# Kernel optimization log

Hardware: AMD Instinct MI355X
Metric: run time of the kernel (lower is better)

## Reference

```python
import jax, jax.numpy as jnp
import numpy as np

N, E, D, T, R, H = 50000, 400000, 256, 3, 6, 4
DK = D // H          # 64, d_k = out_dim // n_heads
OUT = H * DK         # 256
LN_EPS = 1e-5


def setup_inputs() -> dict:
    key = jax.random.key(0)
    ks = jax.random.split(key, 16)
    std = 0.02  # initializer_range in HGTClassfication._init_weights
    f32 = jnp.float32
    inp = {
        "x": jax.random.normal(ks[0], (N, D), f32),
        "Wk": jax.random.normal(ks[1], (T, D, OUT), f32) * std,
        "bk": jnp.zeros((T, OUT), f32),
        "Wq": jax.random.normal(ks[2], (T, D, OUT), f32) * std,
        "bq": jnp.zeros((T, OUT), f32),
        "Wv": jax.random.normal(ks[3], (T, D, OUT), f32) * std,
        "bv": jnp.zeros((T, OUT), f32),
        "Wa": jax.random.normal(ks[4], (T, OUT, OUT), f32) * std,
        "ba": jnp.zeros((T, OUT), f32),
        "rel_pri": jnp.ones((R, H), f32),
        "rel_att": jax.random.normal(ks[5], (R, H, DK, DK), f32) * (1.0 / np.sqrt(DK)),
        "rel_msg": jax.random.normal(ks[6], (R, H, DK, DK), f32) * (1.0 / np.sqrt(DK)),
        "skip": jnp.ones((T,), f32),
        "ln_g": jnp.ones((T, OUT), f32),
        "ln_b": jnp.zeros((T, OUT), f32),
        "node_type": jax.random.randint(ks[7], (N,), 0, T),
        "edge_src": jax.random.randint(ks[8], (E,), 0, N),
        "edge_dst": jax.random.randint(ks[9], (E,), 0, N),
        "edge_type": jax.random.randint(ks[10], (E,), 0, R),
        "n_heads": H,
    }
    return inp


def reference(x, Wk, bk, Wq, bq, Wv, bv, Wa, ba, rel_pri, rel_att, rel_msg,
              skip, ln_g, ln_b, node_type, edge_src, edge_dst, edge_type, n_heads):
    n, d = x.shape
    r, h = rel_pri.shape
    dk = rel_att.shape[-1]
    out_dim = h * dk
    ar = jnp.arange(n)

    def typed_linear(inp_, W, b):
        # per-node-type Linear: compute for all T types, pick by node_type
        y = jnp.einsum('ni,tio->tno', inp_, W) + b[:, None, :]
        return y[node_type, ar]

    k = typed_linear(x, Wk, bk).reshape(n, h, dk)
    q = typed_linear(x, Wq, bq).reshape(n, h, dk)
    v = typed_linear(x, Wv, bv).reshape(n, h, dk)

    # relation-specific transforms (done on nodes, gathered per edge: N*R << E*R work)
    k_rel = jnp.einsum('nhd,rhde->rnhe', k, rel_att)   # [R,N,H,dk]
    v_rel = jnp.einsum('nhd,rhde->rnhe', v, rel_msg)   # [R,N,H,dk]
    key_e = k_rel[edge_type, edge_src]                 # [E,H,dk]
    val_e = v_rel[edge_type, edge_src]                 # [E,H,dk]

    att = (q[edge_dst] * key_e).sum(-1) * rel_pri[edge_type] / jnp.sqrt(jnp.float32(dk))  # [E,H]

    # per-(dst, etype) mailbox softmax + weighted sum (DGL reduce per canonical etype)
    seg = edge_dst * r + edge_type
    S = n * r
    amax = jax.ops.segment_max(att, seg, num_segments=S)
    amax = jax.lax.stop_gradient(jnp.where(jnp.isfinite(amax), amax, 0.0))
    ex = jnp.exp(att - amax[seg])
    denom = jax.ops.segment_sum(ex, seg, num_segments=S)
    w = ex / denom[seg]                                # [E,H]
    hsum = jax.ops.segment_sum(w[:, :, None] * val_e, seg, num_segments=S)  # [S,H,dk]
    cnt = jax.ops.segment_sum(jnp.ones((seg.shape[0],), x.dtype), seg, num_segments=S)

    # cross_reducer='mean' over relations that delivered messages
    t_rel = hsum.reshape(n, r, out_dim)
    present = cnt.reshape(n, r) > 0
    nrel = jnp.maximum(present.sum(-1), 1).astype(x.dtype)
    t = (t_rel * present[..., None].astype(x.dtype)).sum(1) / nrel[:, None]

    trans = typed_linear(t, Wa, ba)
    alpha = jax.nn.sigmoid(skip)[node_type][:, None]
    out = trans * alpha + x * (1.0 - alpha)

    mu = out.mean(-1, keepdims=True)
    var = out.var(-1, keepdims=True)
    normed = (out - mu) * jax.lax.rsqrt(var + LN_EPS) * ln_g[node_type] + ln_b[node_type]

    # nodes with no incoming edges keep their input feature (no 't' in DGL data)
    has_msg = present.any(-1)[:, None]
    return jnp.where(has_msg, normed, x)
```

## Files before the change

kernel.cpp:

```cpp
#include <hip/hip_runtime.h>
#include <hip/hip_bf16.h>


#define NN 50000
#define EE 400000
#define TN 3
#define RN 6
#define HN 4
#define SS (NN * RN)
#define NCHUNK 293
#define CD 16
#define LCAP 640

typedef __hip_bfloat16 bf16;
typedef unsigned short u16;
using bf16x8 = __attribute__((ext_vector_type(8))) __bf16;
using f32x4  = __attribute__((ext_vector_type(4))) float;

__device__ __forceinline__ float b2f(bf16 h) { return __bfloat162float(h); }
__device__ __forceinline__ float busf(u16 u) { return __uint_as_float((unsigned)u << 16); }
__device__ __forceinline__ float blo(unsigned u) { return __uint_as_float(u << 16); }
__device__ __forceinline__ float bhi(unsigned u) { return __uint_as_float(u & 0xffff0000u); }
__device__ __forceinline__ u16 f2us(float f) {
    unsigned u = __float_as_uint(f);
    return (u16)((u + 0x7fffu + ((u >> 16) & 1u)) >> 16);
}
__device__ __forceinline__ float ld(const void* p, long i, int f) {
    return f ? ((const float*)p)[i] : b2f(((const bf16*)p)[i]);
}

__global__ __launch_bounds__(256) void detect_dtype(const void* __restrict__ x,
                                                    int* __restrict__ flag) {
    __shared__ int cnt_s;
    if (threadIdx.x == 0) cnt_s = 0;
    __syncthreads();
    const u16* p = (const u16*)x;
    int c = 0;
    for (int i = threadIdx.x; i < 8192; i += 256) {
        int expo = (p[i] >> 7) & 0xFF;
        if (expo >= 0x97) ++c;
    }
    atomicAdd(&cnt_s, c);
    __syncthreads();
    if (threadIdx.x == 0) *flag = (cnt_s > 64) ? 1 : 0;
}

__global__ __launch_bounds__(256) void prep(const void* __restrict__ rel_att,
        const void* __restrict__ rel_msg,
        const void* __restrict__ Wk, const void* __restrict__ Wq,
        const void* __restrict__ Wv, const void* __restrict__ Wa,
        const void* __restrict__ x, const int* __restrict__ node_type,
        const int* __restrict__ edst, const int* __restrict__ etype,
        const int* __restrict__ flag,
        u16* __restrict__ MTa, u16* __restrict__ MTm,
        u16* __restrict__ WallT, u16* __restrict__ WaT,
        u16* __restrict__ xb,
        int* __restrict__ lists, int* __restrict__ cnts,
        unsigned* __restrict__ cnt) {
    int b = blockIdx.x;
    int t = threadIdx.x;
    if (b < 48) {
        int f = *flag;
        int m = b;
        long base = (long)(m % 24) * 4096;
        if (m < 24) {
            for (int it = 0; it < 16; ++it) {
                int idx = it * 256 + t;
                MTa[base + idx] = f2us(ld(rel_att, base + idx, f));
            }
        } else {
            for (int it = 0; it < 16; ++it) {
                int idx = it * 256 + t;
                int d = idx >> 6, j = idx & 63;
                MTm[base + (j << 6) + d] = f2us(ld(rel_msg, base + idx, f));
            }
        }
    } else if (b < 3120) {
        int f = *flag;
        int m = b - 48;
        if (m < 2304) {
            int ty = m / 768, o3 = m % 768;
            int sec = o3 >> 8, o = o3 & 255;
            const void* W = (sec == 0) ? Wk : (sec == 1) ? Wq : Wv;
            WallT[(size_t)ty * 768 * 256 + (size_t)o3 * 256 + t] =
                f2us(ld(W, (long)ty * 65536 + (long)t * 256 + o, f));
        } else {
            int mm = m - 2304;
            int ty = mm / 256, o = mm % 256;
            WaT[(size_t)ty * 65536 + (size_t)o * 256 + t] =
                f2us(ld(Wa, (long)ty * 65536 + (long)t * 256 + o, f));
        }
    } else if (b < 15620) {
        int f = *flag;
        long i = ((long)(b - 3120) * 256 + t) * 4;
        if (i < (long)NN * 256) {
            if (f) {
                float4 v = *(const float4*)((const float*)x + i);
                ushort4 p; p.x = f2us(v.x); p.y = f2us(v.y); p.z = f2us(v.z); p.w = f2us(v.w);
                *(ushort4*)(xb + i) = p;
            } else {
                *(ushort4*)(xb + i) = *(const ushort4*)((const u16*)x + i);
            }
        }
    } else if (b < 15816) {
        __shared__ int lc[TN], lbase[TN];
        if (t < TN) lc[t] = 0;
        __syncthreads();
        int n = (b - 15620) * 256 + t;
        int pos = -1, ty = 0;
        if (n < NN) {
            ty = node_type[n];
            pos = atomicAdd(&lc[ty], 1);
        }
        __syncthreads();
        if (t < TN) lbase[t] = atomicAdd(&cnts[t], lc[t]);
        __syncthreads();
        if (n < NN) lists[ty * NN + lbase[ty] + pos] = n;
    } else {
        int e = (b - 15816) * 256 + t;
        if (e < EE) atomicAdd(&cnt[etype[e] * NN + edst[e]], 1u);
    }
}

__global__ __launch_bounds__(256) void scanA(const unsigned* __restrict__ cnt,
                                             unsigned* __restrict__ csums) {
    __shared__ unsigned s[256];
    int b = blockIdx.x, t = threadIdx.x;
    int s0 = b * 1024 + t * 4;
    unsigned v = 0;
    if (s0 + 3 < SS) { uint4 u = *(const uint4*)&cnt[s0]; v = u.x + u.y + u.z + u.w; }
    else { for (int j = 0; j < 4; ++j) if (s0 + j < SS) v += cnt[s0 + j]; }
    s[t] = v;
    __syncthreads();
    for (int st = 128; st > 0; st >>= 1) {
        if (t < st) s[t] += s[t + st];
        __syncthreads();
    }
    if (t == 0) csums[b] = s[0];
}

__global__ __launch_bounds__(256) void scanB(unsigned* __restrict__ csums,
                                             int* __restrict__ base) {
    __shared__ unsigned s[512];
    int t = threadIdx.x;
    unsigned a = (t < NCHUNK) ? csums[t] : 0u;
    unsigned b = (256 + t < NCHUNK) ? csums[256 + t] : 0u;
    s[t] = a; s[256 + t] = b;
    __syncthreads();
    for (int st = 1; st < 512; st <<= 1) {
        unsigned x0 = (t >= st) ? s[t - st] : 0u;
        unsigned x1 = (256 + t >= st) ? s[256 + t - st] : 0u;
        __syncthreads();
        s[t] += x0; s[256 + t] += x1;
        __syncthreads();
    }
    if (t < NCHUNK) csums[t] = s[t] - a;
    if (256 + t < NCHUNK) csums[256 + t] = s[256 + t] - b;
    if (t == 0) base[SS] = (int)s[NCHUNK - 1];
}

__global__ __launch_bounds__(256) void scanC(const unsigned* __restrict__ cnt,
        const unsigned* __restrict__ csums, int* __restrict__ base) {
    __shared__ unsigned s[256];
    int b = blockIdx.x, t = threadIdx.x;
    int s0 = b * 1024 + t * 4;
    unsigned vs[4] = {0u, 0u, 0u, 0u};
    if (s0 + 3 < SS) { uint4 u = *(const uint4*)&cnt[s0]; vs[0]=u.x; vs[1]=u.y; vs[2]=u.z; vs[3]=u.w; }
    else { for (int j = 0; j < 4; ++j) if (s0 + j < SS) vs[j] = cnt[s0 + j]; }
    unsigned v = vs[0] + vs[1] + vs[2] + vs[3];
    s[t] = v;
    __syncthreads();
    for (int st = 1; st < 256; st <<= 1) {
        unsigned x = (t >= st) ? s[t - st] : 0u;
        __syncthreads();
        s[t] += x;
        __syncthreads();
    }
    unsigned run = csums[b] + s[t] - v;
    for (int j = 0; j < 4; ++j) {
        if (s0 + j < SS) { base[s0 + j] = (int)run; run += vs[j]; }
    }
}

__global__ __launch_bounds__(256) void scatter_edges(const int* __restrict__ edst,
        const int* __restrict__ etype, const int* __restrict__ base,
        unsigned* __restrict__ cnt, int* __restrict__ sorted) {
    int e = blockIdx.x * 256 + threadIdx.x;
    if (e >= EE) return;
    int seg = etype[e] * NN + edst[e];
    unsigned old = atomicSub(&cnt[seg], 1u);
    sorted[base[seg] + (int)old - 1] = e;
}

__global__ __launch_bounds__(512, 2) void k1_mfma(const u16* __restrict__ xb,
        const u16* __restrict__ WallT,
        const void* __restrict__ bk, const void* __restrict__ bq,
        const void* __restrict__ bv,
        const int* __restrict__ lists, const int* __restrict__ cnts,
        const int* __restrict__ flag,
        u16* __restrict__ kb, u16* __restrict__ qb, u16* __restrict__ vb) {
    int f = *flag;
    int tt = blockIdx.x % TN, tile = blockIdx.x / TN;
    int cnt = cnts[tt];
    int start = tile * 64;
    if (start >= cnt) return;
    __shared__ int nl[64];
    __shared__ __align__(16) u16 xs[64][280];
    __shared__ __align__(16) float bias_s[768];
    int t = threadIdx.x;
    if (t < 64) nl[t] = (start + t < cnt) ? lists[tt * NN + start + t] : -1;
    if (t < 256) {
        bias_s[t]       = ld(bk, tt * 256 + t, f);
        bias_s[256 + t] = ld(bq, tt * 256 + t, f);
        bias_s[512 + t] = ld(bv, tt * 256 + t, f);
    }
    __syncthreads();
    {
        int i = t >> 4, g = t & 15;
        #pragma unroll
        for (int i2 = 0; i2 < 2; ++i2) {
            int row = i + i2 * 32;
            int node = nl[row];
            uint4 a = {0, 0, 0, 0}, b = {0, 0, 0, 0};
            if (node >= 0) {
                const uint4* src = (const uint4*)(xb + (size_t)node * 256 + g * 16);
                a = src[0]; b = src[1];
            }
            *(uint4*)&xs[row][g * 16] = a;
            *(uint4*)&xs[row][g * 16 + 8] = b;
        }
    }
    __syncthreads();
    int w = t >> 6, lane = t & 63, ln = lane & 15, quad = lane >> 4;
    const u16* Wt = WallT + (size_t)tt * 768 * 256;
    f32x4 acc[6][4];
    #pragma unroll
    for (int j = 0; j < 6; ++j)
        #pragma unroll
        for (int g = 0; g < 4; ++g)
            acc[j][g] = (f32x4){0.f, 0.f, 0.f, 0.f};
    for (int kt = 0; kt < 8; ++kt) {
        bf16x8 A[6];
        #pragma unroll
        for (int jt = 0; jt < 6; ++jt)
            A[jt] = *(const bf16x8*)(Wt + (size_t)(w * 96 + jt * 16 + ln) * 256 + kt * 32 + quad * 8);
        bf16x8 B[4];
        #pragma unroll
        for (int g = 0; g < 4; ++g)
            B[g] = *(const bf16x8*)&xs[g * 16 + ln][kt * 32 + quad * 8];
        #pragma unroll
        for (int jt = 0; jt < 6; ++jt)
            #pragma unroll
            for (int g = 0; g < 4; ++g)
                acc[jt][g] = __builtin_amdgcn_mfma_f32_16x16x32_bf16(A[jt], B[g], acc[jt][g], 0, 0, 0);
    }
    #pragma unroll
    for (int jt = 0; jt < 6; ++jt) {
        int jc = w * 96 + jt * 16 + quad * 4;
        float4 bi = *(const float4*)&bias_s[jc];
        int sec = jc >> 8, o = jc & 255;
        u16* basep = (sec == 0 ? kb : sec == 1 ? qb : vb);
        #pragma unroll
        for (int g = 0; g < 4; ++g) {
            int node = nl[g * 16 + ln];
            if (node >= 0) {
                ushort4 p;
                p.x = f2us(acc[jt][g][0] + bi.x); p.y = f2us(acc[jt][g][1] + bi.y);
                p.z = f2us(acc[jt][g][2] + bi.z); p.w = f2us(acc[jt][g][3] + bi.w);
                *(ushort4*)(basep + (size_t)node * 256 + o) = p;
            }
        }
    }
}

__global__ __launch_bounds__(256) void k2k4(const u16* __restrict__ kb,
        const u16* __restrict__ qb, const u16* __restrict__ vb,
        const u16* __restrict__ MTa, const u16* __restrict__ MTm,
        const void* __restrict__ rel_pri,
        const int* __restrict__ sorted, const int* __restrict__ base,
        const int* __restrict__ esrc, const int* __restrict__ edst,
        const int* __restrict__ flag,
        u16* __restrict__ attex_g, float* __restrict__ tacc) {
    int f = *flag;
    int c0 = blockIdx.x * CD;
    int nd = min(CD, NN - c0);
    __shared__ float attL[LCAP];
    __shared__ int srcL[LCAP];
    __shared__ float denomL[CD * HN];
    __shared__ int sb_[CD + 1];
    __shared__ __align__(16) u16 qL[CD][264];
    __shared__ __align__(16) u16 qrs[CD][264];
    int t = threadIdx.x;
    int w = t >> 6, lane = t & 63, ln = lane & 15, quad = lane >> 4;
    {
        int i = t >> 4, g = t & 15;
        uint4 a0 = {0,0,0,0}, a1 = {0,0,0,0};
        if (i < nd) {
            const uint4* src = (const uint4*)(qb + (size_t)(c0 + i) * 256 + g * 16);
            a0 = src[0]; a1 = src[1];
        }
        *(uint4*)&qL[i][g * 16] = a0;
        *(uint4*)&qL[i][g * 16 + 8] = a1;
    }
    f32x4 accF[4];
    #pragma unroll
    for (int m = 0; m < 4; ++m) accF[m] = (f32x4){0.f, 0.f, 0.f, 0.f};

    for (int r = 0; r < RN; ++r) {
        if (t < CD * HN) denomL[t] = 0.f;
        if (t <= nd) sb_[t] = base[r * NN + c0 + t];
        __syncthreads();
        long mtbase = (long)(r * HN + w) * 4096;
        {
            bf16x8 B0 = *(const bf16x8*)&qL[ln][w * 64 + quad * 8];
            bf16x8 B1 = *(const bf16x8*)&qL[ln][w * 64 + quad * 8 + 32];
            #pragma unroll
            for (int mt = 0; mt < 4; ++mt) {
                const u16* ap = MTa + mtbase + (mt * 16 + ln) * 64 + quad * 8;
                bf16x8 A0 = *(const bf16x8*)(ap);
                bf16x8 A1 = *(const bf16x8*)(ap + 32);
                f32x4 acc = {0.f, 0.f, 0.f, 0.f};
                acc = __builtin_amdgcn_mfma_f32_16x16x32_bf16(A0, B0, acc, 0, 0, 0);
                acc = __builtin_amdgcn_mfma_f32_16x16x32_bf16(A1, B1, acc, 0, 0, 0);
                int jc = w * 64 + mt * 16 + quad * 4;
                ushort4 pq;
                pq.x = f2us(acc[0]); pq.y = f2us(acc[1]);
                pq.z = f2us(acc[2]); pq.w = f2us(acc[3]);
                *(ushort4*)&qrs[ln][jc] = pq;
            }
        }
        __syncthreads();
        int b0 = sb_[0], nE = sb_[nd] - b0;
        for (int i = t; i < nE * 4; i += 256) {
            int ei = i >> 2;
            int e = sorted[b0 + ei];
            int h = i & 3;
            int s = esrc[e], dv = edst[e] - c0;
            if (h == 0 && ei < LCAP) srcL[ei] = s;
            const uint4* kp = (const uint4*)(kb + (size_t)s * 256 + h * 64);
            const uint4* qp = (const uint4*)&qrs[dv][h * 64];
            float dot = 0.f;
            #pragma unroll
            for (int ii = 0; ii < 8; ++ii) {
                uint4 a = kp[ii], b = qp[ii];
                dot += blo(a.x) * blo(b.x) + bhi(a.x) * bhi(b.x);
                dot += blo(a.y) * blo(b.y) + bhi(a.y) * bhi(b.y);
                dot += blo(a.z) * blo(b.z) + bhi(a.z) * bhi(b.z);
                dot += blo(a.w) * blo(b.w) + bhi(a.w) * bhi(b.w);
            }
            float attv = dot * ld(rel_pri, r * HN + h, f) * 0.125f;
            attv = fminf(fmaxf(attv, -50.f), 50.f);
            float ex = expf(attv);
            if (i < LCAP) attL[i] = ex;
            else attex_g[(size_t)b0 * 4 + i] = f2us(ex);
            atomicAdd(&denomL[dv * HN + h], ex);
        }
        __syncthreads();
        {
            int half = lane >> 5, lane32 = lane & 31;
            int h = lane32 >> 3;
            for (int i2 = w * 2 + half; i2 < nd; i2 += 8) {
                int sb = sb_[i2], se = sb_[i2 + 1];
                float a0=0.f,a1=0.f,a2=0.f,a3=0.f,a4=0.f,a5=0.f,a6=0.f,a7=0.f;
                if (se > sb) {
                    float inv = 1.f / denomL[i2 * HN + h];
                    for (int idx = sb; idx < se; ++idx) {
                        int rel = idx - b0;
                        int li2 = rel * 4 + h;
                        float wgt = ((li2 < LCAP) ? attL[li2]
                                     : busf(attex_g[(size_t)idx * 4 + h])) * inv;
                        int s = (rel < LCAP) ? srcL[rel] : esrc[sorted[idx]];
                        uint4 v = *(const uint4*)(vb + (size_t)s * 256 + lane32 * 8);
                        a0 += wgt * blo(v.x); a1 += wgt * bhi(v.x);
                        a2 += wgt * blo(v.y); a3 += wgt * bhi(v.y);
                        a4 += wgt * blo(v.z); a5 += wgt * bhi(v.z);
                        a6 += wgt * blo(v.w); a7 += wgt * bhi(v.w);
                    }
                }
                u16 pv8[8];
                pv8[0]=f2us(a0); pv8[1]=f2us(a1); pv8[2]=f2us(a2); pv8[3]=f2us(a3);
                pv8[4]=f2us(a4); pv8[5]=f2us(a5); pv8[6]=f2us(a6); pv8[7]=f2us(a7);
                *(uint4*)&qrs[i2][lane32 * 8] = *(const uint4*)pv8;
            }
        }
        __syncthreads();
        {
            bf16x8 B0 = *(const bf16x8*)&qrs[ln][w * 64 + quad * 8];
            bf16x8 B1 = *(const bf16x8*)&qrs[ln][w * 64 + quad * 8 + 32];
            #pragma unroll
            for (int mt = 0; mt < 4; ++mt) {
                const u16* mp = MTm + mtbase + (mt * 16 + ln) * 64 + quad * 8;
                bf16x8 A0 = *(const bf16x8*)(mp);
                bf16x8 A1 = *(const bf16x8*)(mp + 32);
                accF[mt] = __builtin_amdgcn_mfma_f32_16x16x32_bf16(A0, B0, accF[mt], 0, 0, 0);
                accF[mt] = __builtin_amdgcn_mfma_f32_16x16x32_bf16(A1, B1, accF[mt], 0, 0, 0);
            }
        }
    }
    if (ln < nd) {
        #pragma unroll
        for (int mt = 0; mt < 4; ++mt) {
            int jc = w * 64 + mt * 16 + quad * 4;
            float4 v = {accF[mt][0], accF[mt][1], accF[mt][2], accF[mt][3]};
            *(float4*)(tacc + (long)(c0 + ln) * 256 + jc) = v;
        }
    }
}

__global__ __launch_bounds__(512, 4) void k5_fused(const void* __restrict__ x,
        const float* __restrict__ tacc, const u16* __restrict__ WaT,
        const void* __restrict__ ba, const void* __restrict__ skip,
        const void* __restrict__ ln_g, const void* __restrict__ ln_b,
        const int* __restrict__ base,
        const int* __restrict__ lists, const int* __restrict__ cnts,
        const int* __restrict__ flag, void* out) {
    int f = *flag;
    int tt = blockIdx.x % TN, tile = blockIdx.x / TN;
    int cnt = cnts[tt];
    int start = tile * 64;
    if (start >= cnt) return;
    __shared__ int nl[64];
    __shared__ float invs[64];
    __shared__ int hasv[64];
    __shared__ __align__(16) u16 xs[64][280];
    __shared__ __align__(16) float ba_s[256], lnG_s[256], lnB_s[256];
    __shared__ float red1[64][8], red2[64][8];
    __shared__ float mu_[64], rs_[64];
    int t = threadIdx.x;
    if (t < 64) {
        int node = (start + t < cnt) ? lists[tt * NN + start + t] : -1;
        nl[t] = node;
        int nrel = 0;
        if (node >= 0) {
            #pragma unroll
            for (int r = 0; r < RN; ++r)
                nrel += (base[r * NN + node + 1] > base[r * NN + node]) ? 1 : 0;
        }
        hasv[t] = nrel;
        invs[t] = (nrel > 0) ? 1.f / (float)nrel : 1.f;
    }
    if (t < 256) {
        ba_s[t]  = ld(ba,   tt * 256 + t, f);
        lnG_s[t] = ld(ln_g, tt * 256 + t, f);
        lnB_s[t] = ld(ln_b, tt * 256 + t, f);
    }
    __syncthreads();
    {
        int i = t >> 3, g8 = t & 7;
        int node = nl[i];
        float inv = invs[i];
        int o0 = g8 * 32;
        u16 tmp[32];
        if (node >= 0) {
            const float* src = tacc + (long)node * 256 + o0;
            #pragma unroll
            for (int j = 0; j < 8; ++j) {
                float4 v = *(const float4*)(src + j * 4);
                tmp[j*4+0] = f2us(v.x * inv); tmp[j*4+1] = f2us(v.y * inv);
                tmp[j*4+2] = f2us(v.z * inv); tmp[j*4+3] = f2us(v.w * inv);
            }
        } else {
            #pragma unroll
            for (int j = 0; j < 32; ++j) tmp[j] = 0;
        }
        #pragma unroll
        for (int j = 0; j < 4; ++j)
            *(uint4*)&xs[i][o0 + j * 8] = ((const uint4*)tmp)[j];
    }
    __syncthreads();
    int w = t >> 6, lane = t & 63, ln = lane & 15, quad = lane >> 4;
    const u16* Wt = WaT + (size_t)tt * 65536;
    f32x4 acc[2][4];
    #pragma unroll
    for (int j = 0; j < 2; ++j)
        #pragma unroll
        for (int g = 0; g < 4; ++g)
            acc[j][g] = (f32x4){0.f, 0.f, 0.f, 0.f};
    for (int kt = 0; kt < 8; ++kt) {
        bf16x8 A[2];
        #pragma unroll
        for (int jt = 0; jt < 2; ++jt)
            A[jt] = *(const bf16x8*)(Wt + (size_t)(w * 32 + jt * 16 + ln) * 256 + kt * 32 + quad * 8);
        bf16x8 B[4];
        #pragma unroll
        for (int g = 0; g < 4; ++g)
            B[g] = *(const bf16x8*)&xs[g * 16 + ln][kt * 32 + quad * 8];
        #pragma unroll
        for (int jt = 0; jt < 2; ++jt)
            #pragma unroll
            for (int g = 0; g < 4; ++g)
                acc[jt][g] = __builtin_amdgcn_mfma_f32_16x16x32_bf16(A[jt], B[g], acc[jt][g], 0, 0, 0);
    }
    float sk = ld(skip, tt, f);
    float alpha = 1.f / (1.f + expf(-sk));
    float p1[4] = {0.f, 0.f, 0.f, 0.f}, p2[4] = {0.f, 0.f, 0.f, 0.f};
    #pragma unroll
    for (int g = 0; g < 4; ++g) {
        int node = nl[g * 16 + ln];
        if (node < 0) continue;
        #pragma unroll
        for (int jt = 0; jt < 2; ++jt) {
            int jc = w * 32 + jt * 16 + quad * 4;
            float4 bi = *(const float4*)&ba_s[jc];
            long xo = (long)node * 256 + jc;
            float xv[4];
            if (f) {
                float4 v = *(const float4*)((const float*)x + xo);
                xv[0] = v.x; xv[1] = v.y; xv[2] = v.z; xv[3] = v.w;
            } else {
                ushort4 v = *(const ushort4*)((const u16*)x + xo);
                xv[0] = busf(v.x); xv[1] = busf(v.y); xv[2] = busf(v.z); xv[3] = busf(v.w);
            }
            #pragma unroll
            for (int rg = 0; rg < 4; ++rg) {
                float ov = acc[jt][g][rg] + ((const float*)&bi)[rg];
                ov = ov * alpha + xv[rg] * (1.f - alpha);
                acc[jt][g][rg] = ov;
                p1[g] += ov; p2[g] += ov * ov;
            }
        }
    }
    #pragma unroll
    for (int g = 0; g < 4; ++g) {
        p1[g] += __shfl_xor(p1[g], 16); p1[g] += __shfl_xor(p1[g], 32);
        p2[g] += __shfl_xor(p2[g], 16); p2[g] += __shfl_xor(p2[g], 32);
    }
    if (quad == 0) {
        #pragma unroll
        for (int g = 0; g < 4; ++g) {
            red1[g * 16 + ln][w] = p1[g];
            red2[g * 16 + ln][w] = p2[g];
        }
    }
    __syncthreads();
    if (t < 64) {
        float s1 = 0.f, s2 = 0.f;
        #pragma unroll
        for (int j = 0; j < 8; ++j) { s1 += red1[t][j]; s2 += red2[t][j]; }
        float mu = s1 * (1.f / 256.f);
        float ms = s2 * (1.f / 256.f);
        float var = fmaxf(ms - mu * mu, 0.f);
        mu_[t] = mu; rs_[t] = rsqrtf(var + 1e-5f);
    }
    __syncthreads();
    #pragma unroll
    for (int g = 0; g < 4; ++g) {
        int li = g * 16 + ln;
        int node = nl[li];
        if (node < 0) continue;
        if (hasv[li] > 0) {
            float mu = mu_[li], rs = rs_[li];
            #pragma unroll
            for (int jt = 0; jt < 2; ++jt) {
                int jc = w * 32 + jt * 16 + quad * 4;
                float4 gg = *(const float4*)&lnG_s[jc];
                float4 bb = *(const float4*)&lnB_s[jc];
                long oo = (long)node * 256 + jc;
                float r0 = (acc[jt][g][0] - mu) * rs * gg.x + bb.x;
                float r1 = (acc[jt][g][1] - mu) * rs * gg.y + bb.y;
                float r2 = (acc[jt][g][2] - mu) * rs * gg.z + bb.z;
                float r3 = (acc[jt][g][3] - mu) * rs * gg.w + bb.w;
                if (f) { float4 v = {r0, r1, r2, r3}; *(float4*)((float*)out + oo) = v; }
                else   { ushort4 v; v.x = f2us(r0); v.y = f2us(r1); v.z = f2us(r2); v.w = f2us(r3);
                         *(ushort4*)((u16*)out + oo) = v; }
            }
        } else {
            #pragma unroll
            for (int jt = 0; jt < 2; ++jt) {
                int jc = w * 32 + jt * 16 + quad * 4;
                long oo = (long)node * 256 + jc;
                if (f) { *(float4*)((float*)out + oo) = *(const float4*)((const float*)x + oo); }
                else   { *(ushort4*)((u16*)out + oo) = *(const ushort4*)((const u16*)x + oo); }
            }
        }
    }
}

extern "C" void kernel_launch(void* const* d_in, const int* in_sizes, int n_in,
                              void* d_out, int out_size, void* d_ws, size_t ws_size,
                              hipStream_t stream) {
    const void* x       = d_in[0];
    const void* Wk      = d_in[1];
    const void* bk      = d_in[2];
    const void* Wq      = d_in[3];
    const void* bq      = d_in[4];
    const void* Wv      = d_in[5];
    const void* bv      = d_in[6];
    const void* Wa      = d_in[7];
    const void* ba      = d_in[8];
    const void* rel_pri = d_in[9];
    const void* rel_att = d_in[10];
    const void* rel_msg = d_in[11];
    const void* skip    = d_in[12];
    const void* ln_g    = d_in[13];
    const void* ln_b    = d_in[14];
    const int* node_type = (const int*)d_in[15];
    const int* edge_src  = (const int*)d_in[16];
    const int* edge_dst  = (const int*)d_in[17];
    const int* edge_type = (const int*)d_in[18];
    char* w = (char*)d_ws;

    u16*      kb     = (u16*)(w);
    u16*      qb     = (u16*)(w + 25600000);
    u16*      vb     = (u16*)(w + 51200000);
    float*    tacc   = (float*)(w + 76800000);
    u16*      xb     = (u16*)(w + 76800000);
    u16*      attex  = (u16*)(w + 128000000);
    int*      sorted = (int*)(w + 131200000);
    int*      base   = (int*)(w + 132800000);
    int*      nlists = (int*)(w + 134000064);
    u16*      MTa    = (u16*)(w + 134600064);
    u16*      MTm    = (u16*)(w + 134796672);
    u16*      WallT  = (u16*)(w + 134993280);
    u16*      WaT    = (u16*)(w + 136172928);
    unsigned* cnt    = (unsigned*)(w + 136566144);
    int*      ncnts  = (int*)(w + 137766144);
    int*      flag   = (int*)(w + 137766208);
    unsigned* csums  = (unsigned*)(w + 137766272);

    hipMemsetAsync(w + 136566144, 0, 1201408, stream);

    detect_dtype<<<dim3(1), dim3(256), 0, stream>>>(x, flag);
    prep<<<dim3(17379), dim3(256), 0, stream>>>(
        rel_att, rel_msg, Wk, Wq, Wv, Wa, x, node_type, edge_dst, edge_type,
        flag, MTa, MTm, WallT, WaT, xb, nlists, ncnts, cnt);
    scanA<<<dim3(NCHUNK), dim3(256), 0, stream>>>(cnt, csums);
    scanB<<<dim3(1), dim3(256), 0, stream>>>(csums, base);
    scanC<<<dim3(NCHUNK), dim3(256), 0, stream>>>(cnt, csums, base);
    scatter_edges<<<dim3((EE + 255) / 256), dim3(256), 0, stream>>>(
        edge_dst, edge_type, base, cnt, sorted);

    k1_mfma<<<dim3(TN * ((NN + 63) / 64)), dim3(512), 0, stream>>>(
        xb, WallT, bk, bq, bv, nlists, ncnts, flag, kb, qb, vb);


    k2k4<<<dim3(NN / CD), dim3(256), 0, stream>>>(
        kb, qb, vb, MTa, MTm, rel_pri, sorted, base, edge_src, edge_dst,
        flag, attex, tacc);

    k5_fused<<<dim3(TN * ((NN + 63) / 64)), dim3(512), 0, stream>>>(
        x, tacc, WaT, ba, skip, ln_g, ln_b, base, nlists, ncnts, flag, d_out);
}
```

Before: 588.6 us.

## Fuse edge attention scoring into aggregation loop with shuffle-reduced dot products

Replaces the separate edge-scoring pass (per-edge dot products, exp, LDS/global staging, atomic denominators) with a single loop per destination node. Each 8-lane group computes its head's q·k dot product and reduces it with shuffles, accumulates exp-weighted V and the denominator in registers, and normalizes at the end. This removes the attention buffers, the shared atomics, one barrier and the global spill path for large blocks. The cost is that the k and v rows are loaded in the same serial dependent loop, and the exp and shuffles now sit on the aggregation critical path.

```diff
diff --git a/kernel.cpp b/kernel.cpp
--- a/kernel.cpp
+++ b/kernel.cpp
@@ -10,7 +10,6 @@
 #define SS (NN * RN)
 #define NCHUNK 293
 #define CD 16
-#define LCAP 640
 
 typedef __hip_bfloat16 bf16;
 typedef unsigned short u16;
@@ -278,20 +277,19 @@
         const u16* __restrict__ MTa, const u16* __restrict__ MTm,
         const void* __restrict__ rel_pri,
         const int* __restrict__ sorted, const int* __restrict__ base,
-        const int* __restrict__ esrc, const int* __restrict__ edst,
-        const int* __restrict__ flag,
-        u16* __restrict__ attex_g, float* __restrict__ tacc) {
+        const int* __restrict__ esrc,
+        const int* __restrict__ flag, float* __restrict__ tacc) {
     int f = *flag;
     int c0 = blockIdx.x * CD;
     int nd = min(CD, NN - c0);
-    __shared__ float attL[LCAP];
-    __shared__ int srcL[LCAP];
-    __shared__ float denomL[CD * HN];
     __shared__ int sb_[CD + 1];
     __shared__ __align__(16) u16 qL[CD][264];
-    __shared__ __align__(16) u16 qrs[CD][264];
+    __shared__ __align__(16) u16 qrelL[CD][264];
+    __shared__ __align__(16) u16 srawL[CD][264];
     int t = threadIdx.x;
     int w = t >> 6, lane = t & 63, ln = lane & 15, quad = lane >> 4;
+    int half = lane >> 5, lane32 = lane & 31;
+    int hh = lane32 >> 3;
     {
         int i = t >> 4, g = t & 15;
         uint4 a0 = {0,0,0,0}, a1 = {0,0,0,0};
@@ -307,7 +305,6 @@
     for (int m = 0; m < 4; ++m) accF[m] = (f32x4){0.f, 0.f, 0.f, 0.f};
 
     for (int r = 0; r < RN; ++r) {
-        if (t < CD * HN) denomL[t] = 0.f;
         if (t <= nd) sb_[t] = base[r * NN + c0 + t];
         __syncthreads();
         long mtbase = (long)(r * HN + w) * 4096;
@@ -326,67 +323,51 @@
                 ushort4 pq;
                 pq.x = f2us(acc[0]); pq.y = f2us(acc[1]);
                 pq.z = f2us(acc[2]); pq.w = f2us(acc[3]);
-                *(ushort4*)&qrs[ln][jc] = pq;
-            }
-        }
-        __syncthreads();
-        int b0 = sb_[0], nE = sb_[nd] - b0;
-        for (int i = t; i < nE * 4; i += 256) {
-            int ei = i >> 2;
-            int e = sorted[b0 + ei];
-            int h = i & 3;
-            int s = esrc[e], dv = edst[e] - c0;
-            if (h == 0 && ei < LCAP) srcL[ei] = s;
-            const uint4* kp = (const uint4*)(kb + (size_t)s * 256 + h * 64);
-            const uint4* qp = (const uint4*)&qrs[dv][h * 64];
-            float dot = 0.f;
-            #pragma unroll
-            for (int ii = 0; ii < 8; ++ii) {
-                uint4 a = kp[ii], b = qp[ii];
-                dot += blo(a.x) * blo(b.x) + bhi(a.x) * bhi(b.x);
-                dot += blo(a.y) * blo(b.y) + bhi(a.y) * bhi(b.y);
-                dot += blo(a.z) * blo(b.z) + bhi(a.z) * bhi(b.z);
-                dot += blo(a.w) * blo(b.w) + bhi(a.w) * bhi(b.w);
-            }
-            float attv = dot * ld(rel_pri, r * HN + h, f) * 0.125f;
-            attv = fminf(fmaxf(attv, -50.f), 50.f);
-            float ex = expf(attv);
-            if (i < LCAP) attL[i] = ex;
-            else attex_g[(size_t)b0 * 4 + i] = f2us(ex);
-            atomicAdd(&denomL[dv * HN + h], ex);
+                *(ushort4*)&qrelL[ln][jc] = pq;
+            }
         }
         __syncthreads();
         {
-            int half = lane >> 5, lane32 = lane & 31;
-            int h = lane32 >> 3;
+            float pri = ld(rel_pri, r * HN + hh, f) * 0.125f;
             for (int i2 = w * 2 + half; i2 < nd; i2 += 8) {
                 int sb = sb_[i2], se = sb_[i2 + 1];
                 float a0=0.f,a1=0.f,a2=0.f,a3=0.f,a4=0.f,a5=0.f,a6=0.f,a7=0.f;
                 if (se > sb) {
-                    float inv = 1.f / denomL[i2 * HN + h];
+                    uint4 qv = *(const uint4*)&qrelL[i2][lane32 * 8];
+                    float q0=blo(qv.x),q1=bhi(qv.x),q2=blo(qv.y),q3=bhi(qv.y);
+                    float q4=blo(qv.z),q5=bhi(qv.z),q6=blo(qv.w),q7=bhi(qv.w);
+                    float den = 0.f;
                     for (int idx = sb; idx < se; ++idx) {
-                        int rel = idx - b0;
-                        int li2 = rel * 4 + h;
-                        float wgt = ((li2 < LCAP) ? attL[li2]
-                                     : busf(attex_g[(size_t)idx * 4 + h])) * inv;
-                        int s = (rel < LCAP) ? srcL[rel] : esrc[sorted[idx]];
-                        uint4 v = *(const uint4*)(vb + (size_t)s * 256 + lane32 * 8);
-                        a0 += wgt * blo(v.x); a1 += wgt * bhi(v.x);
-                        a2 += wgt * blo(v.y); a3 += wgt * bhi(v.y);
-                        a4 += wgt * blo(v.z); a5 += wgt * bhi(v.z);
-                        a6 += wgt * blo(v.w); a7 += wgt * bhi(v.w);
+                        int e = sorted[idx];
+                        int s = esrc[e];
+                        size_t rowoff = (size_t)s * 256 + lane32 * 8;
+                        uint4 kv = *(const uint4*)(kb + rowoff);
+                        uint4 vv = *(const uint4*)(vb + rowoff);
+                        float d = blo(kv.x)*q0 + bhi(kv.x)*q1 + blo(kv.y)*q2 + bhi(kv.y)*q3
+                                + blo(kv.z)*q4 + bhi(kv.z)*q5 + blo(kv.w)*q6 + bhi(kv.w)*q7;
+                        d += __shfl_xor(d, 1); d += __shfl_xor(d, 2); d += __shfl_xor(d, 4);
+                        float attv = fminf(fmaxf(d * pri, -50.f), 50.f);
+                        float ex = expf(attv);
+                        den += ex;
+                        a0 += ex * blo(vv.x); a1 += ex * bhi(vv.x);
+                        a2 += ex * blo(vv.y); a3 += ex * bhi(vv.y);
+                        a4 += ex * blo(vv.z); a5 += ex * bhi(vv.z);
+                        a6 += ex * blo(vv.w); a7 += ex * bhi(vv.w);
                     }
+                    float inv = 1.f / den;
+                    a0 *= inv; a1 *= inv; a2 *= inv; a3 *= inv;
+                    a4 *= inv; a5 *= inv; a6 *= inv; a7 *= inv;
                 }
                 u16 pv8[8];
                 pv8[0]=f2us(a0); pv8[1]=f2us(a1); pv8[2]=f2us(a2); pv8[3]=f2us(a3);
                 pv8[4]=f2us(a4); pv8[5]=f2us(a5); pv8[6]=f2us(a6); pv8[7]=f2us(a7);
-                *(uint4*)&qrs[i2][lane32 * 8] = *(const uint4*)pv8;
+                *(uint4*)&srawL[i2][lane32 * 8] = *(const uint4*)pv8;
             }
         }
         __syncthreads();
         {
-            bf16x8 B0 = *(const bf16x8*)&qrs[ln][w * 64 + quad * 8];
-            bf16x8 B1 = *(const bf16x8*)&qrs[ln][w * 64 + quad * 8 + 32];
+            bf16x8 B0 = *(const bf16x8*)&srawL[ln][w * 64 + quad * 8];
+            bf16x8 B1 = *(const bf16x8*)&srawL[ln][w * 64 + quad * 8 + 32];
             #pragma unroll
             for (int mt = 0; mt < 4; ++mt) {
                 const u16* mp = MTm + mtbase + (mt * 16 + ln) * 64 + quad * 8;
@@ -617,6 +598,7 @@
     int*      ncnts  = (int*)(w + 137766144);
     int*      flag   = (int*)(w + 137766208);
     unsigned* csums  = (unsigned*)(w + 137766272);
+    (void)attex;
 
     hipMemsetAsync(w + 136566144, 0, 1201408, stream);
 
@@ -635,8 +617,8 @@
 
 
     k2k4<<<dim3(NN / CD), dim3(256), 0, stream>>>(
-        kb, qb, vb, MTa, MTm, rel_pri, sorted, base, edge_src, edge_dst,
-        flag, attex, tacc);
+        kb, qb, vb, MTa, MTm, rel_pri, sorted, base, edge_src,
+        flag, tacc);
 
     k5_fused<<<dim3(TN * ((NN + 63) / 64)), dim3(512), 0, stream>>>(
         x, tacc, WaT, ba, skip, ln_g, ln_b, base, nlists, ncnts, flag, d_out);
```

After: 591.6 us. Within noise of the previous version (+0.5%).
